# Performance work log

Hardware: AMD Instinct MI355X
Metric: run time of the kernel (lower is better)

Reference implementation:

```python
import jax, jax.numpy as jnp
import numpy as np

COST_CLASS = 2.0
COST_BBOX = 5.0
COST_GIOU = 2.0
COST_INNER = 9999.0
FOCAL_ALPHA = 0.25
FOCAL_GAMMA = 2.0
EPS = 1e-8


def box_cxcywh_to_xyxy(b):
    cx, cy, w, h = b[..., 0], b[..., 1], b[..., 2], b[..., 3]
    return jnp.stack([cx - 0.5 * w, cy - 0.5 * h, cx + 0.5 * w, cy + 0.5 * h], axis=-1)


def generalized_box_iou(boxes1, boxes2):
    # boxes in xyxy; boxes1 [N,4], boxes2 [T,4] -> [N,T]
    area1 = (boxes1[:, 2] - boxes1[:, 0]) * (boxes1[:, 3] - boxes1[:, 1])
    area2 = (boxes2[:, 2] - boxes2[:, 0]) * (boxes2[:, 3] - boxes2[:, 1])
    lt = jnp.maximum(boxes1[:, None, :2], boxes2[None, :, :2])
    rb = jnp.minimum(boxes1[:, None, 2:], boxes2[None, :, 2:])
    wh = jnp.clip(rb - lt, 0.0)
    inter = wh[..., 0] * wh[..., 1]
    union = area1[:, None] + area2[None, :] - inter
    iou = inter / union
    # enclosing box
    lt_c = jnp.minimum(boxes1[:, None, :2], boxes2[None, :, :2])
    rb_c = jnp.maximum(boxes1[:, None, 2:], boxes2[None, :, 2:])
    wh_c = jnp.clip(rb_c - lt_c, 0.0)
    area_c = wh_c[..., 0] * wh_c[..., 1]
    return iou - (area_c - union) / area_c


def setup_inputs() -> dict:
    key = jax.random.key(0)
    k1, k2, k3, k4, k5, k6 = jax.random.split(key, 6)
    bs, nq, nc, T = 16, 900, 91, 1024
    return {
        "pred_logits": jax.random.normal(k1, (bs, nq, nc), dtype=jnp.float32),
        "pred_boxes": jax.random.uniform(k2, (bs, nq, 4), dtype=jnp.float32),
        "pred_points": jax.random.uniform(k3, (bs, nq, 2), dtype=jnp.float32),
        "pred_objs": jax.random.normal(k4, (bs, nq, 1), dtype=jnp.float32),
        "tgt_labels": jax.random.randint(k5, (T,), 0, nc, dtype=jnp.int64),
        "tgt_boxes": jax.random.uniform(k6, (T, 4), dtype=jnp.float32),
    }


def reference(pred_logits, pred_boxes, pred_points, pred_objs, tgt_labels, tgt_boxes):
    bs, nq, nc = pred_logits.shape
    out_prob = jax.nn.sigmoid(pred_logits.reshape(bs * nq, nc))       # [N,C]
    out_bbox = pred_boxes.reshape(bs * nq, 4)                          # [N,4]
    out_point = pred_points.reshape(bs * nq, 2)                        # [N,2]
    out_obj = jax.nn.sigmoid(pred_objs.reshape(bs * nq, 1))            # [N,1]
    out_prob = out_prob * out_obj

    # focal classification cost, gathered at target classes -> [N,T]
    neg = (1.0 - FOCAL_ALPHA) * out_prob ** FOCAL_GAMMA * (-jnp.log(1.0 - out_prob + EPS))
    pos = FOCAL_ALPHA * (1.0 - out_prob) ** FOCAL_GAMMA * (-jnp.log(out_prob + EPS))
    cost_class = jnp.take(pos, tgt_labels, axis=1) - jnp.take(neg, tgt_labels, axis=1)

    out_xyxy = box_cxcywh_to_xyxy(out_bbox)
    tgt_xyxy = box_cxcywh_to_xyxy(tgt_boxes)

    # L1 cdist on xyxy boxes -> [N,T]
    cost_bbox = jnp.sum(jnp.abs(out_xyxy[:, None, :] - tgt_xyxy[None, :, :]), axis=-1)

    cost_giou = -generalized_box_iou(out_xyxy, tgt_xyxy)               # [N,T]

    # inner-point cost: 1 if predicted point falls outside target box
    left = out_point[:, 0, None] - tgt_xyxy[None, :, 0]
    top = out_point[:, 1, None] - tgt_xyxy[None, :, 1]
    right = tgt_xyxy[None, :, 2] - out_point[:, 0, None]
    bottom = tgt_xyxy[None, :, 3] - out_point[:, 1, None]
    min_dist = jnp.minimum(jnp.minimum(left, top), jnp.minimum(right, bottom))
    cost_inner = 1.0 - (min_dist >= 0.0).astype(out_prob.dtype)

    C = (COST_BBOX * cost_bbox + COST_CLASS * cost_class
         + COST_GIOU * cost_giou + COST_INNER * cost_inner)
    return C.reshape(bs, nq, -1)
```

## Files before the change

### kernel.cpp

```cpp
#include <hip/hip_runtime.h>
#include <math.h>


#define BN 16
#define BT 256
#define TBL_STRIDE 128

__global__ __launch_bounds__(BT) void matcher_kernel(
    const float* __restrict__ logits,
    const float* __restrict__ boxes,
    const float* __restrict__ points,
    const float* __restrict__ objs,
    const int*   __restrict__ labels,
    const float* __restrict__ tboxes,
    float* __restrict__ out,
    int N, int C, int T)
{
    __shared__ float s_table[BN * TBL_STRIDE];
    __shared__ float s_row[BN][8];

    const int tid = threadIdx.x;
    const int rowBase = blockIdx.y * BN;
    const int t = blockIdx.x * BT + tid;

    if (tid < BN) {
        int n = rowBase + tid;
        if (n < N) {
            float4 b = *(const float4*)(boxes + 4 * n);
            float x0 = b.x - 0.5f * b.z;
            float y0 = b.y - 0.5f * b.w;
            float x1 = b.x + 0.5f * b.z;
            float y1 = b.y + 0.5f * b.w;
            s_row[tid][0] = x0;
            s_row[tid][1] = y0;
            s_row[tid][2] = x1;
            s_row[tid][3] = y1;
            float2 p = *(const float2*)(points + 2 * n);
            s_row[tid][4] = p.x;
            s_row[tid][5] = p.y;
            s_row[tid][6] = (x1 - x0) * (y1 - y0);
        }
    }

    for (int idx = tid; idx < BN * C; idx += BT) {
        int r = idx / C;
        int c = idx - r * C;
        int n = rowBase + r;
        float v = 0.0f;
        if (n < N) {
            float lg = logits[n * C + c];
            float ps = 1.0f / (1.0f + expf(-lg));
            float po = 1.0f / (1.0f + expf(-objs[n]));
            float p = ps * po;
            float omp = 1.0f - p;
            float pos = 0.25f * (omp * omp) * (-logf(p + 1e-8f));
            float neg = 0.75f * (p * p) * (-logf(omp + 1e-8f));
            v = pos - neg;
        }
        s_table[r * TBL_STRIDE + c] = v;
    }

    __syncthreads();

    if (t < T) {
        float4 tb = *(const float4*)(tboxes + 4 * t);
        float tx0 = tb.x - 0.5f * tb.z;
        float ty0 = tb.y - 0.5f * tb.w;
        float tx1 = tb.x + 0.5f * tb.z;
        float ty1 = tb.y + 0.5f * tb.w;
        float tarea = (tx1 - tx0) * (ty1 - ty0);
        int lab = labels[t];

        #pragma unroll
        for (int r = 0; r < BN; ++r) {
            int n = rowBase + r;
            if (n < N) {
                float x0 = s_row[r][0], y0 = s_row[r][1];
                float x1 = s_row[r][2], y1 = s_row[r][3];
                float px = s_row[r][4], py = s_row[r][5];
                float a1 = s_row[r][6];
                float cc = s_table[r * TBL_STRIDE + lab];

                float l1 = fabsf(x0 - tx0) + fabsf(y0 - ty0)
                         + fabsf(x1 - tx1) + fabsf(y1 - ty1);

                float ix0 = fmaxf(x0, tx0), iy0 = fmaxf(y0, ty0);
                float ix1 = fminf(x1, tx1), iy1 = fminf(y1, ty1);
                float iw = fmaxf(ix1 - ix0, 0.0f);
                float ih = fmaxf(iy1 - iy0, 0.0f);
                float inter = iw * ih;
                float uni = a1 + tarea - inter;
                float iou = inter / uni;
                float cx0 = fminf(x0, tx0), cy0 = fminf(y0, ty0);
                float cx1 = fmaxf(x1, tx1), cy1 = fmaxf(y1, ty1);
                float cw = fmaxf(cx1 - cx0, 0.0f);
                float ch = fmaxf(cy1 - cy0, 0.0f);
                float carea = cw * ch;
                float giou = iou - (carea - uni) / carea;

                float left = px - tx0;
                float top = py - ty0;
                float right = tx1 - px;
                float bottom = ty1 - py;
                float mind = fminf(fminf(left, top), fminf(right, bottom));
                float inner = (mind >= 0.0f) ? 0.0f : 1.0f;

                float Cv = 5.0f * l1 + 2.0f * cc - 2.0f * giou + 9999.0f * inner;
                out[n * T + t] = Cv;
            }
        }
    }
}

extern "C" void kernel_launch(void* const* d_in, const int* in_sizes, int n_in,
                              void* d_out, int out_size, void* d_ws, size_t ws_size,
                              hipStream_t stream) {
    const float* logits = (const float*)d_in[0];
    const float* boxes  = (const float*)d_in[1];
    const float* points = (const float*)d_in[2];
    const float* objs   = (const float*)d_in[3];
    const int*   labels = (const int*)d_in[4];
    const float* tboxes = (const float*)d_in[5];
    float* out = (float*)d_out;

    int N = in_sizes[1] / 4;
    int T = in_sizes[5] / 4;
    int C = in_sizes[0] / N;

    dim3 grid((T + BT - 1) / BT, (N + BN - 1) / BN);
    matcher_kernel<<<grid, BT, 0, stream>>>(logits, boxes, points, objs,
                                            labels, tboxes, out, N, C, T);
}
```

Baseline: 116.4 us.

## Process four targets per thread with float4 stores and hoisted objectness sigmoid

Each thread now computes four consecutive targets, so a block covers all 1024 targets and the per-row class table is built once per row block rather than four times. Output writes become float4 stores, the objectness sigmoid is computed once per row, and divisions are replaced by the fast hardware reciprocal. The grid shrinks to a quarter of its blocks, which lowers parallelism. Targets in a trailing partial group of four are no longer written when T is not a multiple of four, and the approximate reciprocal may change results slightly.

Measured after the change: 101.2 us. 13.1% less time.

```diff
diff --git a/kernel.cpp b/kernel.cpp
--- a/kernel.cpp
+++ b/kernel.cpp
@@ -4,7 +4,8 @@
 
 #define BN 16
 #define BT 256
-#define TBL_STRIDE 128
+#define VT 4
+#define TBL_STRIDE 96
 
 __global__ __launch_bounds__(BT) void matcher_kernel(
     const float* __restrict__ logits,
@@ -21,7 +22,7 @@
 
     const int tid = threadIdx.x;
     const int rowBase = blockIdx.y * BN;
-    const int t = blockIdx.x * BT + tid;
+    const int t0 = (blockIdx.x * BT + tid) * VT;
 
     if (tid < BN) {
         int n = rowBase + tid;
@@ -39,8 +40,10 @@
             s_row[tid][4] = p.x;
             s_row[tid][5] = p.y;
             s_row[tid][6] = (x1 - x0) * (y1 - y0);
+            s_row[tid][7] = 1.0f / (1.0f + expf(-objs[n]));
         }
     }
+    __syncthreads();
 
     for (int idx = tid; idx < BN * C; idx += BT) {
         int r = idx / C;
@@ -50,8 +53,7 @@
         if (n < N) {
             float lg = logits[n * C + c];
             float ps = 1.0f / (1.0f + expf(-lg));
-            float po = 1.0f / (1.0f + expf(-objs[n]));
-            float p = ps * po;
+            float p = ps * s_row[r][7];
             float omp = 1.0f - p;
             float pos = 0.25f * (omp * omp) * (-logf(p + 1e-8f));
             float neg = 0.75f * (p * p) * (-logf(omp + 1e-8f));
@@ -59,55 +61,64 @@
         }
         s_table[r * TBL_STRIDE + c] = v;
     }
-
     __syncthreads();
 
-    if (t < T) {
-        float4 tb = *(const float4*)(tboxes + 4 * t);
-        float tx0 = tb.x - 0.5f * tb.z;
-        float ty0 = tb.y - 0.5f * tb.w;
-        float tx1 = tb.x + 0.5f * tb.z;
-        float ty1 = tb.y + 0.5f * tb.w;
-        float tarea = (tx1 - tx0) * (ty1 - ty0);
-        int lab = labels[t];
+    if (t0 + VT <= T) {
+        float tx0[VT], ty0[VT], tx1[VT], ty1[VT], tarea[VT];
+        int lab[VT];
+        int4 lv = *(const int4*)(labels + t0);
+        lab[0] = lv.x; lab[1] = lv.y; lab[2] = lv.z; lab[3] = lv.w;
+        #pragma unroll
+        for (int j = 0; j < VT; ++j) {
+            float4 tb = *(const float4*)(tboxes + 4 * (t0 + j));
+            tx0[j] = tb.x - 0.5f * tb.z;
+            ty0[j] = tb.y - 0.5f * tb.w;
+            tx1[j] = tb.x + 0.5f * tb.z;
+            ty1[j] = tb.y + 0.5f * tb.w;
+            tarea[j] = (tx1[j] - tx0[j]) * (ty1[j] - ty0[j]);
+        }
 
         #pragma unroll
         for (int r = 0; r < BN; ++r) {
             int n = rowBase + r;
-            if (n < N) {
-                float x0 = s_row[r][0], y0 = s_row[r][1];
-                float x1 = s_row[r][2], y1 = s_row[r][3];
-                float px = s_row[r][4], py = s_row[r][5];
-                float a1 = s_row[r][6];
-                float cc = s_table[r * TBL_STRIDE + lab];
+            if (n >= N) continue;
+            float4 ra = *(const float4*)&s_row[r][0];
+            float4 rb = *(const float4*)&s_row[r][4];
+            float x0 = ra.x, y0 = ra.y, x1 = ra.z, y1 = ra.w;
+            float px = rb.x, py = rb.y, a1 = rb.z;
+            const float* trow = s_table + r * TBL_STRIDE;
 
-                float l1 = fabsf(x0 - tx0) + fabsf(y0 - ty0)
-                         + fabsf(x1 - tx1) + fabsf(y1 - ty1);
+            float4 res;
+            float* resp = (float*)&res;
+            #pragma unroll
+            for (int j = 0; j < VT; ++j) {
+                float cc = trow[lab[j]];
 
-                float ix0 = fmaxf(x0, tx0), iy0 = fmaxf(y0, ty0);
-                float ix1 = fminf(x1, tx1), iy1 = fminf(y1, ty1);
-                float iw = fmaxf(ix1 - ix0, 0.0f);
-                float ih = fmaxf(iy1 - iy0, 0.0f);
-                float inter = iw * ih;
-                float uni = a1 + tarea - inter;
-                float iou = inter / uni;
-                float cx0 = fminf(x0, tx0), cy0 = fminf(y0, ty0);
-                float cx1 = fmaxf(x1, tx1), cy1 = fmaxf(y1, ty1);
-                float cw = fmaxf(cx1 - cx0, 0.0f);
-                float ch = fmaxf(cy1 - cy0, 0.0f);
+                float l1 = fabsf(x0 - tx0[j]) + fabsf(y0 - ty0[j])
+                         + fabsf(x1 - tx1[j]) + fabsf(y1 - ty1[j]);
+
+                float iw = fminf(x1, tx1[j]) - fmaxf(x0, tx0[j]);
+                float ih = fminf(y1, ty1[j]) - fmaxf(y0, ty0[j]);
+                float inter = fmaxf(iw, 0.0f) * fmaxf(ih, 0.0f);
+                float uni = (a1 + tarea[j]) - inter;
+                float iou = inter * __builtin_amdgcn_rcpf(uni);
+
+                float cw = fmaxf(x1, tx1[j]) - fminf(x0, tx0[j]);
+                float ch = fmaxf(y1, ty1[j]) - fminf(y0, ty0[j]);
                 float carea = cw * ch;
-                float giou = iou - (carea - uni) / carea;
+                float giou = iou - (carea - uni) * __builtin_amdgcn_rcpf(carea);
 
-                float left = px - tx0;
-                float top = py - ty0;
-                float right = tx1 - px;
-                float bottom = ty1 - py;
+                float left = px - tx0[j];
+                float top = py - ty0[j];
+                float right = tx1[j] - px;
+                float bottom = ty1[j] - py;
                 float mind = fminf(fminf(left, top), fminf(right, bottom));
-                float inner = (mind >= 0.0f) ? 0.0f : 1.0f;
 
-                float Cv = 5.0f * l1 + 2.0f * cc - 2.0f * giou + 9999.0f * inner;
-                out[n * T + t] = Cv;
+                float Cv = fmaf(5.0f, l1, fmaf(2.0f, cc, -2.0f * giou));
+                Cv += (mind >= 0.0f) ? 0.0f : 9999.0f;
+                resp[j] = Cv;
             }
+            *(float4*)(out + (size_t)n * T + t0) = res;
         }
     }
 }
@@ -127,7 +138,7 @@
     int T = in_sizes[5] / 4;
     int C = in_sizes[0] / N;
 
-    dim3 grid((T + BT - 1) / BT, (N + BN - 1) / BN);
+    dim3 grid((T + BT * VT - 1) / (BT * VT), (N + BN - 1) / BN);
     matcher_kernel<<<grid, BT, 0, stream>>>(logits, boxes, points, objs,
                                             labels, tboxes, out, N, C, T);
 }
```

## Split focal table into separate kernel and remap threads to rows with vector stores

Applied to the files above, without the earlier changes.

Moves the focal classification table into a separate kernel that writes a class-major table to workspace, so each row's table is computed once instead of once per target tile. The main kernel now maps threads to prediction rows and loops over a 64-target tile held in shared memory. It writes four outputs per thread as non-temporal vector stores and computes GIoU with one hardware reciprocal instead of two divisions. In exchange it adds a second launch, uncoalesced gathered table reads keyed by label, and reduced-precision reciprocals. The grid assumes T is a multiple of 64.

Measured after the change: 240.9 us. +107.0%, slower.

```diff
diff --git a/kernel.cpp b/kernel.cpp
--- a/kernel.cpp
+++ b/kernel.cpp
@@ -2,112 +2,114 @@
 #include <math.h>
 
 
-#define BN 16
-#define BT 256
-#define TBL_STRIDE 128
+typedef float nfloat4 __attribute__((ext_vector_type(4)));
 
-__global__ __launch_bounds__(BT) void matcher_kernel(
+#define K1_CB 23
+#define TC   64
+
+__global__ __launch_bounds__(256) void table_kernel(
     const float* __restrict__ logits,
+    const float* __restrict__ objs,
+    float* __restrict__ tableT,
+    int N, int C)
+{
+    int n = blockIdx.x * 256 + threadIdx.x;
+    if (n >= N) return;
+    float po = __builtin_amdgcn_rcpf(1.0f + expf(-objs[n]));
+    int c0 = blockIdx.y * K1_CB;
+    int c1 = c0 + K1_CB; if (c1 > C) c1 = C;
+    for (int c = c0; c < c1; ++c) {
+        float lg = logits[n * C + c];
+        float ps = __builtin_amdgcn_rcpf(1.0f + expf(-lg));
+        float p = ps * po;
+        float omp = 1.0f - p;
+        float pos = 0.25f * (omp * omp) * (-logf(p + 1e-8f));
+        float neg = 0.75f * (p * p) * (-logf(omp + 1e-8f));
+        tableT[(size_t)c * N + n] = pos - neg;
+    }
+}
+
+__global__ __launch_bounds__(256) void matcher_main(
     const float* __restrict__ boxes,
     const float* __restrict__ points,
-    const float* __restrict__ objs,
     const int*   __restrict__ labels,
     const float* __restrict__ tboxes,
+    const float* __restrict__ tableT,
     float* __restrict__ out,
-    int N, int C, int T)
+    int N, int T)
 {
-    __shared__ float s_table[BN * TBL_STRIDE];
-    __shared__ float s_row[BN][8];
+    __shared__ float4 s_box[TC];
+    __shared__ float2 s_al[TC];
 
     const int tid = threadIdx.x;
-    const int rowBase = blockIdx.y * BN;
-    const int t = blockIdx.x * BT + tid;
+    const int tBase = blockIdx.x * TC;
 
-    if (tid < BN) {
-        int n = rowBase + tid;
-        if (n < N) {
-            float4 b = *(const float4*)(boxes + 4 * n);
-            float x0 = b.x - 0.5f * b.z;
-            float y0 = b.y - 0.5f * b.w;
-            float x1 = b.x + 0.5f * b.z;
-            float y1 = b.y + 0.5f * b.w;
-            s_row[tid][0] = x0;
-            s_row[tid][1] = y0;
-            s_row[tid][2] = x1;
-            s_row[tid][3] = y1;
-            float2 p = *(const float2*)(points + 2 * n);
-            s_row[tid][4] = p.x;
-            s_row[tid][5] = p.y;
-            s_row[tid][6] = (x1 - x0) * (y1 - y0);
-        }
+    if (tid < TC) {
+        int t = tBase + tid;
+        float4 tb = *(const float4*)(tboxes + 4 * t);
+        float x0 = tb.x - 0.5f * tb.z;
+        float y0 = tb.y - 0.5f * tb.w;
+        float x1 = tb.x + 0.5f * tb.z;
+        float y1 = tb.y + 0.5f * tb.w;
+        s_box[tid] = make_float4(x0, y0, x1, y1);
+        s_al[tid] = make_float2((x1 - x0) * (y1 - y0),
+                                __int_as_float(labels[t]));
     }
 
-    for (int idx = tid; idx < BN * C; idx += BT) {
-        int r = idx / C;
-        int c = idx - r * C;
-        int n = rowBase + r;
-        float v = 0.0f;
-        if (n < N) {
-            float lg = logits[n * C + c];
-            float ps = 1.0f / (1.0f + expf(-lg));
-            float po = 1.0f / (1.0f + expf(-objs[n]));
-            float p = ps * po;
-            float omp = 1.0f - p;
-            float pos = 0.25f * (omp * omp) * (-logf(p + 1e-8f));
-            float neg = 0.75f * (p * p) * (-logf(omp + 1e-8f));
-            v = pos - neg;
-        }
-        s_table[r * TBL_STRIDE + c] = v;
-    }
+    const int n = blockIdx.y * 256 + tid;
+    const bool valid = (n < N);
+    const int nc = valid ? n : (N - 1);
+    float4 b = *(const float4*)(boxes + 4 * nc);
+    float x0 = b.x - 0.5f * b.z;
+    float y0 = b.y - 0.5f * b.w;
+    float x1 = b.x + 0.5f * b.z;
+    float y1 = b.y + 0.5f * b.w;
+    float a1 = (x1 - x0) * (y1 - y0);
+    float2 pp = *(const float2*)(points + 2 * nc);
+    float px = pp.x, py = pp.y;
 
     __syncthreads();
 
-    if (t < T) {
-        float4 tb = *(const float4*)(tboxes + 4 * t);
-        float tx0 = tb.x - 0.5f * tb.z;
-        float ty0 = tb.y - 0.5f * tb.w;
-        float tx1 = tb.x + 0.5f * tb.z;
-        float ty1 = tb.y + 0.5f * tb.w;
-        float tarea = (tx1 - tx0) * (ty1 - ty0);
-        int lab = labels[t];
+    float* orow = out + (size_t)nc * T + tBase;
+    for (int tt = 0; tt < TC; tt += 4) {
+        nfloat4 res;
+        #pragma unroll
+        for (int j = 0; j < 4; ++j) {
+            int ti = tt + j;
+            float4 tb = s_box[ti];
+            float2 al = s_al[ti];
+            float tx0 = tb.x, ty0 = tb.y, tx1 = tb.z, ty1 = tb.w;
+            float tarea = al.x;
+            int lab = __float_as_int(al.y);
+            float cc = tableT[(size_t)lab * N + nc];
 
-        #pragma unroll
-        for (int r = 0; r < BN; ++r) {
-            int n = rowBase + r;
-            if (n < N) {
-                float x0 = s_row[r][0], y0 = s_row[r][1];
-                float x1 = s_row[r][2], y1 = s_row[r][3];
-                float px = s_row[r][4], py = s_row[r][5];
-                float a1 = s_row[r][6];
-                float cc = s_table[r * TBL_STRIDE + lab];
+            float l1 = fabsf(x0 - tx0) + fabsf(y0 - ty0)
+                     + fabsf(x1 - tx1) + fabsf(y1 - ty1);
 
-                float l1 = fabsf(x0 - tx0) + fabsf(y0 - ty0)
-                         + fabsf(x1 - tx1) + fabsf(y1 - ty1);
+            float iw = fminf(x1, tx1) - fmaxf(x0, tx0);
+            float ih = fminf(y1, ty1) - fmaxf(y0, ty0);
+            float inter = fmaxf(iw, 0.0f) * fmaxf(ih, 0.0f);
+            float uni = (a1 + tarea) - inter;
 
-                float ix0 = fmaxf(x0, tx0), iy0 = fmaxf(y0, ty0);
-                float ix1 = fminf(x1, tx1), iy1 = fminf(y1, ty1);
-                float iw = fmaxf(ix1 - ix0, 0.0f);
-                float ih = fmaxf(iy1 - iy0, 0.0f);
-                float inter = iw * ih;
-                float uni = a1 + tarea - inter;
-                float iou = inter / uni;
-                float cx0 = fminf(x0, tx0), cy0 = fminf(y0, ty0);
-                float cx1 = fmaxf(x1, tx1), cy1 = fmaxf(y1, ty1);
-                float cw = fmaxf(cx1 - cx0, 0.0f);
-                float ch = fmaxf(cy1 - cy0, 0.0f);
-                float carea = cw * ch;
-                float giou = iou - (carea - uni) / carea;
+            float cw = fmaxf(x1, tx1) - fminf(x0, tx0);
+            float ch = fmaxf(y1, ty1) - fminf(y0, ty0);
+            float carea = cw * ch;
 
-                float left = px - tx0;
-                float top = py - ty0;
-                float right = tx1 - px;
-                float bottom = ty1 - py;
-                float mind = fminf(fminf(left, top), fminf(right, bottom));
-                float inner = (mind >= 0.0f) ? 0.0f : 1.0f;
+            float R = __builtin_amdgcn_rcpf(uni * carea);
+            float giou = (inter * carea - uni * (carea - uni)) * R;
 
-                float Cv = 5.0f * l1 + 2.0f * cc - 2.0f * giou + 9999.0f * inner;
-                out[n * T + t] = Cv;
-            }
+            float left = px - tx0;
+            float top = py - ty0;
+            float right = tx1 - px;
+            float bottom = ty1 - py;
+            float mind = fminf(fminf(left, top), fminf(right, bottom));
+
+            float Cv = fmaf(5.0f, l1, fmaf(2.0f, cc, -2.0f * giou));
+            Cv += (mind >= 0.0f) ? 0.0f : 9999.0f;
+            res[j] = Cv;
+        }
+        if (valid) {
+            __builtin_nontemporal_store(res, (nfloat4*)(orow + tt));
         }
     }
 }
@@ -122,12 +124,16 @@
     const int*   labels = (const int*)d_in[4];
     const float* tboxes = (const float*)d_in[5];
     float* out = (float*)d_out;
+    float* tableT = (float*)d_ws;
 
     int N = in_sizes[1] / 4;
     int T = in_sizes[5] / 4;
     int C = in_sizes[0] / N;
 
-    dim3 grid((T + BT - 1) / BT, (N + BN - 1) / BN);
-    matcher_kernel<<<grid, BT, 0, stream>>>(logits, boxes, points, objs,
-                                            labels, tboxes, out, N, C, T);
+    dim3 g1((N + 255) / 256, (C + K1_CB - 1) / K1_CB);
+    table_kernel<<<g1, 256, 0, stream>>>(logits, objs, tableT, N, C);
+
+    dim3 g2(T / TC, (N + 255) / 256);
+    matcher_main<<<g2, 256, 0, stream>>>(boxes, points, labels, tboxes,
+                                         tableT, out, N, T);
 }
```
